# Performance work log

Measured on AMD Instinct MI355X. Metric: run time of the kernel, lower is better.

## Reference

```python
import jax, jax.numpy as jnp
import numpy as np
import math

B, D, L, Nh, Dk, Dv, K, CONV_NUM = 16, 256, 1024, 8, 32, 32, 7, 4
EPS = 1e-5


def _pos_encoding():
    # matches PosEncoder: freqs/phases per channel, sin(pos*freqs + phases), shape [D, L]
    idx = jnp.arange(D)
    i = idx.astype(jnp.float32)
    even = (idx % 2 == 0)
    freqs = jnp.where(even, 10000.0 ** (-i / D), -(10000.0 ** ((1.0 - i) / D)))
    phases = jnp.where(even, 0.0, math.pi / 2)
    pos = jnp.arange(L, dtype=jnp.float32)
    return jnp.sin(pos[None, :] * freqs[:, None] + phases[:, None])


def _layer_norm(x, g, b):
    # nn.LayerNorm([D, L]) on [B, D, L]: normalize over last two dims
    m = jnp.mean(x, axis=(1, 2), keepdims=True)
    v = jnp.mean((x - m) ** 2, axis=(1, 2), keepdims=True)
    return (x - m) * jax.lax.rsqrt(v + EPS) * g + b


def _ds_conv(x, dw, db, pw, pb):
    # depthwise conv1d (groups=D, same padding) + pointwise 1x1 conv
    y = jax.lax.conv_general_dilated(
        x, dw[:, None, :], window_strides=(1,), padding=[(K // 2, K // 2)],
        feature_group_count=D, dimension_numbers=('NCH', 'OIH', 'NCH'))
    y = y + db[None, :, None]
    return jnp.einsum('bdl,ed->bel', y, pw) + pb[None, :, None]


def setup_inputs() -> dict:
    key = jax.random.key(0)
    ks = jax.random.split(key, 12)

    def n(k, shape, scale):
        return jax.random.normal(k, shape, jnp.float32) * scale

    x = jax.random.normal(ks[0], (B, D, L), jnp.float32)
    mask = jax.random.randint(ks[1], (B, L), 0, 2).astype(jnp.int32)
    dw_w = n(ks[2], (CONV_NUM, D, K), 0.1)
    dw_b = jnp.zeros((CONV_NUM, D), jnp.float32)
    pw_w = n(ks[3], (CONV_NUM, D, D), 0.05)
    pw_b = jnp.zeros((CONV_NUM, D), jnp.float32)
    ln_g = jnp.ones((CONV_NUM + 2, D, L), jnp.float32)
    ln_b = jnp.zeros((CONV_NUM + 2, D, L), jnp.float32)
    Wq = n(ks[4], (Nh, D, Dk), 0.05)
    Wk = n(ks[5], (Nh, D, Dk), 0.05)
    Wv = n(ks[6], (Nh, D, Dv), 0.05)
    Wo = n(ks[7], (D, Dv * Nh), 0.05)
    fc_w = n(ks[8], (D, D), 0.05)
    fc_b = jnp.zeros((D,), jnp.float32)
    return dict(x=x, mask=mask, dw_w=dw_w, dw_b=dw_b, pw_w=pw_w, pw_b=pw_b,
                ln_g=ln_g, ln_b=ln_b, Wq=Wq, Wk=Wk, Wv=Wv, Wo=Wo,
                fc_w=fc_w, fc_b=fc_b)


def reference(x, mask, dw_w, dw_b, pw_w, pw_b, ln_g, ln_b, Wq, Wk, Wv, Wo, fc_w, fc_b):
    m = mask.astype(jnp.float32)  # [B, L]
    out = x + _pos_encoding()[None]
    res = out
    out = _layer_norm(out, ln_g[0], ln_b[0])
    for i in range(CONV_NUM):
        out = jax.nn.relu(_ds_conv(out, dw_w[i], dw_b[i], pw_w[i], pw_b[i])) + res
        # F.dropout in eval mode is identity
        res = out
        out = _layer_norm(out, ln_g[i + 1], ln_b[i + 1])
    # self attention (batched over heads instead of per-head loop; same math)
    xt = out.transpose(0, 2, 1)  # [B, L, D]
    q = jnp.einsum('bld,hdk->bhlk', xt, Wq)
    k = jnp.einsum('bld,hdk->bhlk', xt, Wk)
    v = jnp.einsum('bld,hdv->bhlv', xt, Wv)
    scores = jnp.einsum('bhqk,bhlk->bhql', q, k) * (1.0 / math.sqrt(Dk))
    hm = m[:, None, None, :]  # mask over key dim
    scores = scores * hm + (1.0 - hm) * (-1e30)
    attn = jax.nn.softmax(scores, axis=-1) * m[:, None, :, None]  # zero padded query rows
    heads = jnp.einsum('bhql,bhlv->bqhv', attn, v).reshape(B, L, Nh * Dv)  # head-major concat
    att_out = (heads @ Wo).transpose(0, 2, 1)  # [B, D, L]
    out = att_out + res
    res = out
    out = _layer_norm(out, ln_g[CONV_NUM + 1], ln_b[CONV_NUM + 1])
    out = jnp.einsum('bdl,ed->bel', out, fc_w) + fc_b[None, :, None]  # nn.Linear on [B,L,D]
    out = jax.nn.relu(out) + res
    return out
```

## Files before the change

kernel.cpp:

```cpp
#include <hip/hip_runtime.h>
#include <hip/hip_bf16.h>

#define NB 16
#define ND 256
#define NL 1024
#define NHH 8
#define NDK 32
#define NKW 7
#define NCONV 4
#define NPB (ND*NL)

constexpr float LN_EPS = 1e-5f;

typedef __attribute__((ext_vector_type(4))) float f32x4;
typedef __attribute__((ext_vector_type(4))) short bf16x4;
typedef __attribute__((ext_vector_type(8))) short bf16x8;

__device__ __forceinline__ short bf16s(float f){
  return (short)__builtin_bit_cast(unsigned short, __float2bfloat16(f));
}
__device__ __forceinline__ float b2f(short s){
  return __builtin_bit_cast(float, ((unsigned)(unsigned short)s) << 16);
}

__device__ __forceinline__ void ln_ab(const float* st, int slot, int b, float& mean, float& rstd){
  float s = 0.f, ss = 0.f;
  #pragma unroll
  for(int bin=0;bin<8;bin++){
    const float* p = st + ((size_t)((slot*NB+b)*8+bin))*32;
    s += p[0]; ss += p[1];
  }
  mean = s * (1.0f/NPB);
  float var = ss * (1.0f/NPB) - mean*mean;
  rstd = rsqrtf(var + LN_EPS);
}

__device__ __forceinline__ void stats_reduce(float s, float ss, float* stats, int slot, int b, int bin){
  __shared__ float red[8];
  #pragma unroll
  for(int o=32;o>0;o>>=1){ s += __shfl_down(s,o); ss += __shfl_down(ss,o); }
  int lane = threadIdx.x & 63, w = threadIdx.x >> 6;
  if(lane==0){ red[w*2]=s; red[w*2+1]=ss; }
  __syncthreads();
  if(threadIdx.x==0){
    float* p = stats + ((size_t)((slot*NB+b)*8+bin))*32;
    atomicAdd(&p[0], red[0]+red[2]+red[4]+red[6]);
    atomicAdd(&p[1], red[1]+red[3]+red[5]+red[7]);
  }
}

__global__ __launch_bounds__(256) void k_prep(const float* __restrict__ pw_w, const float* __restrict__ fc_w,
    const float* __restrict__ Wo, const float* __restrict__ Wq, const float* __restrict__ Wk,
    const float* __restrict__ Wv, const float* __restrict__ g, const float* __restrict__ btab,
    short* __restrict__ Wpwb, short* __restrict__ Wfcb, short* __restrict__ Wob, short* __restrict__ Wcat,
    short* __restrict__ gT, short* __restrict__ bT, float* __restrict__ postab){
  __shared__ float T[64][65];
  int blk = blockIdx.x, tid = threadIdx.x;
  if(blk < 256){
    int idx = blk*1024 + tid*4;
    f32x4 v = *(const f32x4*)(pw_w + idx);
    bf16x4 o;
    #pragma unroll
    for(int j=0;j<4;j++) o[j] = bf16s(v[j]);
    *(bf16x4*)(Wpwb + idx) = o;
  } else if(blk < 320){
    int idx = (blk-256)*1024 + tid*4;
    f32x4 v = *(const f32x4*)(fc_w + idx);
    bf16x4 o;
    #pragma unroll
    for(int j=0;j<4;j++) o[j] = bf16s(v[j]);
    *(bf16x4*)(Wfcb + idx) = o;
  } else if(blk < 384){
    int idx = (blk-320)*1024 + tid*4;
    int e = idx >> 8;
    bf16x4 o;
    #pragma unroll
    for(int j=0;j<4;j++){ int d = (idx+j)&255; o[j] = bf16s(Wo[d*ND + e]); }
    *(bf16x4*)(Wob + idx) = o;
  } else if(blk < 576){
    int idx = (blk-384)*1024 + tid*4;
    int og = idx >> 8, d = idx & 255;
    int seg = og >> 8, o = og & 255, h = o >> 5, k = o & 31;
    const float* W = (seg==0) ? Wq : ((seg==1) ? Wk : Wv);
    bf16x4 ov;
    #pragma unroll
    for(int j=0;j<4;j++) ov[j] = bf16s(W[((size_t)(h*ND + d + j))*NDK + k]);
    *(bf16x4*)(Wcat + idx) = ov;
  } else if(blk < 832){
    int d = blk - 576;
    int l = tid*4;
    const float LN1E4_OVER_D = 9.210340371976184f / (float)ND;
    float freq, phase;
    if((d & 1) == 0){ freq =  __expf(-(float)d*LN1E4_OVER_D);      phase = 0.f; }
    else            { freq = -__expf((1.f-(float)d)*LN1E4_OVER_D); phase = 1.5707963267948966f; }
    f32x4 o;
    #pragma unroll
    for(int j=0;j<4;j++) o[j] = sinf((float)(l+j)*freq + phase);
    *(f32x4*)(postab + ((size_t)d<<10) + l) = o;
  } else {
    int blk2 = blk - 832;
    int which = blk2 >> 6;
    int tile = blk2 & 63;
    int d0 = (tile & 3) << 6, l0 = (tile >> 2) << 6;
    const float* src = (which < 6) ? (g + (size_t)which*NPB) : (btab + (size_t)(which-6)*NPB);
    short* dst = (which < 6) ? (gT + (size_t)which*NPB) : (bT + (size_t)(which-6)*NPB);
    for(int i=tid;i<1024;i+=256){
      int dd = i>>4, l4 = i&15;
      f32x4 v = *(const f32x4*)(src + (size_t)(d0+dd)*NL + l0 + l4*4);
      #pragma unroll
      for(int j=0;j<4;j++) T[dd][l4*4+j] = v[j];
    }
    __syncthreads();
    for(int i=tid;i<1024;i+=256){
      int ll = i>>4, d4 = i&15;
      bf16x4 o;
      #pragma unroll
      for(int j=0;j<4;j++) o[j] = bf16s(T[d4*4+j][ll]);
      *(bf16x4*)(dst + (size_t)(l0+ll)*ND + d0 + d4*4) = o;
    }
  }
}

__global__ __launch_bounds__(256) void k_posadd(const float* __restrict__ x, const float* __restrict__ postab,
                                                short* __restrict__ Rb, float* __restrict__ stats){
  int blk = blockIdx.x;
  int lt = blk & 15, dt = (blk>>4)&3, b = blk>>6;
  int l0 = lt*64, d0 = dt*64;
  __shared__ float T[64][65];
  int tid = threadIdx.x;
  for(int i=tid;i<1024;i+=256){
    int dd = i>>4, l4 = i&15;
    int d = d0+dd;
    f32x4 xv = *(const f32x4*)(x + ((size_t)(b*ND+d)<<10) + l0 + l4*4);
    f32x4 pv = *(const f32x4*)(postab + ((size_t)d<<10) + l0 + l4*4);
    #pragma unroll
    for(int j=0;j<4;j++) T[dd][l4*4+j] = xv[j] + pv[j];
  }
  __syncthreads();
  float s=0.f, ss=0.f;
  for(int i=tid;i<1024;i+=256){
    int ll = i>>4, d4 = i&15;
    bf16x4 o;
    #pragma unroll
    for(int j=0;j<4;j++){
      short rs = bf16s(T[d4*4+j][ll]);
      o[j] = rs;
      float rv = b2f(rs);
      s += rv; ss += rv*rv;
    }
    *(bf16x4*)(Rb + ((size_t)(b*NL+l0+ll)<<8) + d0 + d4*4) = o;
  }
  stats_reduce(s, ss, stats, 0, b, blk & 7);
}

__global__ __launch_bounds__(256) void k_dwconvT(const short* __restrict__ Rb, const short* __restrict__ gT,
                                                 const short* __restrict__ bT, const float* __restrict__ w7,
                                                 const float* __restrict__ db, const float* __restrict__ stats,
                                                 short* __restrict__ Y, int slot){
  int blk = blockIdx.x;
  int lblk = blk & 63, b = blk >> 6;
  int tid = threadIdx.x;
  __shared__ float wLds[NKW][ND];
  __shared__ float dbLds[ND];
  for(int i=tid;i<ND*NKW;i+=256){ int d=i/NKW, q=i-d*NKW; wLds[q][d] = w7[i]; }
  dbLds[tid] = db[tid];
  float mean, rstd; ln_ab(stats, slot, b, mean, rstd);
  float mr = mean*rstd;
  __syncthreads();
  int d0 = (tid & 63)*4;
  int l0 = lblk*16 + (tid >> 6)*4;
  f32x4 ln[10];
  #pragma unroll
  for(int i=0;i<10;i++){
    int lp = l0 - 3 + i;
    if(lp >= 0 && lp < NL){
      bf16x4 v = *(const bf16x4*)(Rb + ((size_t)(b*NL+lp)<<8) + d0);
      bf16x4 gv = *(const bf16x4*)(gT + ((size_t)lp<<8) + d0);
      bf16x4 bv = *(const bf16x4*)(bT + ((size_t)lp<<8) + d0);
      f32x4 t;
      #pragma unroll
      for(int j=0;j<4;j++) t[j] = (b2f(v[j])*rstd - mr)*b2f(gv[j]) + b2f(bv[j]);
      ln[i] = t;
    } else ln[i] = (f32x4){0.f,0.f,0.f,0.f};
  }
  f32x4 dbv = *(const f32x4*)(&dbLds[d0]);
  #pragma unroll
  for(int jl=0;jl<4;jl++){
    f32x4 acc = dbv;
    #pragma unroll
    for(int q=0;q<NKW;q++){
      f32x4 wq = *(const f32x4*)(&wLds[q][d0]);
      #pragma unroll
      for(int j=0;j<4;j++) acc[j] += ln[jl+q][j]*wq[j];
    }
    bf16x4 o;
    #pragma unroll
    for(int j=0;j<4;j++) o[j] = bf16s(acc[j]);
    *(bf16x4*)(Y + ((size_t)(b*NL + l0 + jl)<<8) + d0) = o;
  }
}

__device__ __forceinline__ void stage_rows_bf16(short* dst, const short* src, int tid, int c){
  for(int i=tid;i<1024;i+=256){
    int rr = i>>4, kk = i&15;
    bf16x8 w = *(const bf16x8*)(src + (size_t)rr*ND + c*128 + kk*8);
    *(bf16x8*)((char*)dst + rr*256 + ((kk*16) ^ ((rr&7)<<4))) = w;
  }
}
__device__ __forceinline__ void stage_act_lnb(short* dst, const short* src, const short* g, const short* bt,
                                              float mean, float rstd, int tid, int c){
  float mr = mean*rstd;
  for(int i=tid;i<1024;i+=256){
    int ll = i>>4, kk = i&15;
    size_t off = (size_t)ll*ND + c*128 + kk*8;
    bf16x8 v = *(const bf16x8*)(src + off);
    bf16x8 gv = *(const bf16x8*)(g + off);
    bf16x8 bv = *(const bf16x8*)(bt + off);
    bf16x8 o;
    #pragma unroll
    for(int j=0;j<8;j++) o[j] = bf16s((b2f(v[j])*rstd - mr)*b2f(gv[j]) + b2f(bv[j]));
    *(bf16x8*)((char*)dst + ll*256 + ((kk*16) ^ ((ll&7)<<4))) = o;
  }
}
__device__ __forceinline__ void mfma_core(const short* As, const short* Bs, int wm, int wn,
                                          int lq, int gg, f32x4 acc[2][2]){
  #pragma unroll
  for(int t=0;t<4;t++){
    bf16x8 a[2], bb[2];
    #pragma unroll
    for(int m=0;m<2;m++){
      int row = wm*32 + m*16 + lq;
      a[m] = *(const bf16x8*)((const char*)As + row*256 + ((t*64 + gg*16) ^ ((row&7)<<4)));
    }
    #pragma unroll
    for(int n=0;n<2;n++){
      int row = wn*32 + n*16 + lq;
      bb[n] = *(const bf16x8*)((const char*)Bs + row*256 + ((t*64 + gg*16) ^ ((row&7)<<4)));
    }
    #pragma unroll
    for(int m=0;m<2;m++)
      #pragma unroll
      for(int n=0;n<2;n++)
        acc[m][n] = __builtin_amdgcn_mfma_f32_16x16x32_bf16(a[m], bb[n], acc[m][n], 0,0,0);
  }
}

#define GEMM_PROLOGUE() \
  int blk = blockIdx.x; \
  int lt = blk & 15, et = (blk>>4)&3, b = blk>>6; \
  int l0 = lt*64, e0 = et*64; \
  int tid = threadIdx.x; \
  int w = tid>>6, lane = tid&63, lq = lane&15, gg = lane>>4; \
  int wm = w&1, wn = w>>1; \
  __shared__ short As[8192], Bs[8192]; \
  f32x4 acc[2][2]; \
  acc[0][0]=acc[0][1]=acc[1][0]=acc[1][1] = (f32x4){0.f,0.f,0.f,0.f};

__global__ __launch_bounds__(256) void k_pw(const short* __restrict__ Y, const short* __restrict__ Wb,
                                            const float* __restrict__ bias, short* __restrict__ Rb,
                                            float* __restrict__ stats, int slot_out){
  GEMM_PROLOGUE();
  const short* Asrc = Y + ((size_t)(b*NL)+l0)*ND;
  const short* Bsrc = Wb + (size_t)e0*ND;
  for(int c=0;c<2;c++){
    __syncthreads();
    stage_rows_bf16(As, Asrc, tid, c);
    stage_rows_bf16(Bs, Bsrc, tid, c);
    __syncthreads();
    mfma_core(As, Bs, wm, wn, lq, gg, acc);
  }
  float s=0.f, ss=0.f;
  #pragma unroll
  for(int n=0;n<2;n++){
    int e = e0 + wn*32 + n*16 + lq;
    float bv = bias[e];
    #pragma unroll
    for(int m=0;m<2;m++){
      #pragma unroll
      for(int r=0;r<4;r++){
        int l = l0 + wm*32 + m*16 + gg*4 + r;
        size_t ix = (size_t)(b*NL+l)*ND + e;
        float v = fmaxf(acc[m][n][r] + bv, 0.f);
        float rr = b2f(Rb[ix]) + v;
        short rs = bf16s(rr);
        Rb[ix] = rs;
        float r2 = b2f(rs);
        s += r2; ss += r2*r2;
      }
    }
  }
  stats_reduce(s, ss, stats, slot_out, b, blk & 7);
}

__global__ __launch_bounds__(256) void k_qkvf(const short* __restrict__ Rb, const short* __restrict__ gT,
                                              const short* __restrict__ bT, const float* __restrict__ stats,
                                              const short* __restrict__ Wcat, short* __restrict__ Qb,
                                              short* __restrict__ Kb, short* __restrict__ Vb){
  int blk = blockIdx.x;
  int lt = blk & 15;
  int tmp = blk >> 4;
  int et = tmp % 12, b = tmp / 12;
  int l0 = lt*64, e0g = et*64;
  int seg = et >> 2;
  int tid = threadIdx.x;
  int w = tid>>6, lane = tid&63, lq = lane&15, gg = lane>>4;
  int wm = w&1, wn = w>>1;
  __shared__ short As[8192], Bs[8192];
  f32x4 acc[2][2];
  acc[0][0]=acc[0][1]=acc[1][0]=acc[1][1] = (f32x4){0.f,0.f,0.f,0.f};
  float mean, rstd; ln_ab(stats, 4, b, mean, rstd);
  const short* Asrc = Rb + ((size_t)(b*NL)+l0)*ND;
  const short* gs = gT + (size_t)l0*ND;
  const short* bs = bT + (size_t)l0*ND;
  const short* Bsrc = Wcat + (size_t)e0g*ND;
  for(int c=0;c<2;c++){
    __syncthreads();
    stage_act_lnb(As, Asrc, gs, bs, mean, rstd, tid, c);
    stage_rows_bf16(Bs, Bsrc, tid, c);
    __syncthreads();
    mfma_core(As, Bs, wm, wn, lq, gg, acc);
  }
  #pragma unroll
  for(int n=0;n<2;n++){
    int eo = (et&3)*64 + wn*32 + n*16 + lq;
    int h = eo>>5, dk = eo&31;
    if(seg < 2){
      short* outp = (seg==0) ? Qb : Kb;
      #pragma unroll
      for(int m=0;m<2;m++){
        #pragma unroll
        for(int r=0;r<4;r++){
          int l = l0 + wm*32 + m*16 + gg*4 + r;
          outp[((size_t)(b*NHH+h)*NL + l)*NDK + dk] = bf16s(acc[m][n][r]);
        }
      }
    } else {
      #pragma unroll
      for(int m=0;m<2;m++){
        int lb = l0 + wm*32 + m*16 + gg*4;
        bf16x4 pk;
        #pragma unroll
        for(int r=0;r<4;r++) pk[r] = bf16s(acc[m][n][r]);
        *(bf16x4*)(Vb + ((size_t)(b*NHH+h)*NDK + dk)*NL + lb) = pk;
      }
    }
  }
}

__global__ __launch_bounds__(256) void k_attn(const short* __restrict__ Qb, const short* __restrict__ Kb,
                                              const short* __restrict__ Vt, const int* __restrict__ mask,
                                              short* __restrict__ heads){
  int blk = blockIdx.x;
  int qblk = blk >> 7, bh = blk & 127;
  int b = bh >> 3, h = bh & 7;
  int tid = threadIdx.x;
  int w = tid >> 6, lane = tid & 63;
  int lq = lane & 15, gg = lane >> 4;

  __shared__ short Ks[64][40];
  __shared__ short Vs[32*64];
  __shared__ short Ps[4][16][40];
  __shared__ float msh[64];

  int qrow = qblk*64 + w*16 + lq;
  bf16x8 qf = *(const bf16x8*)(Qb + ((size_t)bh*NL + qrow)*NDK + gg*8);

  bf16x8 ones;
  #pragma unroll
  for(int j=0;j<8;j++) ones[j] = (short)0x3F80;

  f32x4 zero = {0.f,0.f,0.f,0.f};
  f32x4 o0 = zero, o1 = zero, o2 = zero;
  const float scale = 0.17677669529663687f;

  for(int t0=0; t0<NL; t0+=64){
    __syncthreads();
    {
      int key = tid >> 2, c = tid & 3;
      *(bf16x8*)(&Ks[key][c*8]) = *(const bf16x8*)(Kb + ((size_t)bh*NL + t0 + key)*NDK + c*8);
      int v = tid >> 3, ch = tid & 7;
      *(bf16x8*)((char*)Vs + v*128 + ((ch*16) ^ ((v&7)<<4))) =
          *(const bf16x8*)(Vt + ((size_t)bh*NDK + v)*NL + t0 + ch*8);
      if(tid < 64) msh[tid] = ((float)mask[b*NL + t0 + tid] - 1.f) * 1e30f;
    }
    __syncthreads();
    #pragma unroll
    for(int sub=0; sub<2; sub++){
      bf16x8 a0 = *(const bf16x8*)(&Ks[sub*32 + lq][gg*8]);
      bf16x8 a1 = *(const bf16x8*)(&Ks[sub*32 + 16 + lq][gg*8]);
      f32x4 c0 = __builtin_amdgcn_mfma_f32_16x16x32_bf16(a0, qf, zero, 0, 0, 0);
      f32x4 c1 = __builtin_amdgcn_mfma_f32_16x16x32_bf16(a1, qf, zero, 0, 0, 0);
      bf16x4 p0, p1;
      #pragma unroll
      for(int r=0;r<4;r++){
        float pv0 = __expf(__builtin_fmaf(c0[r], scale, msh[sub*32 + gg*4 + r]));
        p0[r] = bf16s(pv0);
        float pv1 = __expf(__builtin_fmaf(c1[r], scale, msh[sub*32 + 16 + gg*4 + r]));
        p1[r] = bf16s(pv1);
      }
      *(bf16x4*)(&Ps[w][lq][gg*4])      = p0;
      *(bf16x4*)(&Ps[w][lq][16 + gg*4]) = p1;
      bf16x8 pf = *(const bf16x8*)(&Ps[w][lq][gg*8]);
      int cc = sub*4 + gg;
      bf16x8 b0 = *(const bf16x8*)((const char*)Vs + lq*128      + ((cc*16) ^ ((lq&7)<<4)));
      bf16x8 b1 = *(const bf16x8*)((const char*)Vs + (16+lq)*128 + ((cc*16) ^ (((16+lq)&7)<<4)));
      o0 = __builtin_amdgcn_mfma_f32_16x16x32_bf16(pf, b0, o0, 0, 0, 0);
      o1 = __builtin_amdgcn_mfma_f32_16x16x32_bf16(pf, b1, o1, 0, 0, 0);
      o2 = __builtin_amdgcn_mfma_f32_16x16x32_bf16(pf, ones, o2, 0, 0, 0);
    }
  }
  #pragma unroll
  for(int r=0;r<4;r++){
    int ql = gg*4 + r;
    int qg = qblk*64 + w*16 + ql;
    float mq = (float)mask[b*NL + qg];
    float sc = mq / o2[r];
    short* op = heads + ((size_t)(b*NL + qg))*(NHH*NDK) + h*NDK;
    op[lq]      = bf16s(o0[r]*sc);
    op[16 + lq] = bf16s(o1[r]*sc);
  }
}

__global__ __launch_bounds__(256) void k_wo(const short* __restrict__ H, const short* __restrict__ Wb,
                                            short* __restrict__ Rb, float* __restrict__ stats){
  GEMM_PROLOGUE();
  const short* Asrc = H + ((size_t)(b*NL)+l0)*ND;
  const short* Bsrc = Wb + (size_t)e0*ND;
  for(int c=0;c<2;c++){
    __syncthreads();
    stage_rows_bf16(As, Asrc, tid, c);
    stage_rows_bf16(Bs, Bsrc, tid, c);
    __syncthreads();
    mfma_core(As, Bs, wm, wn, lq, gg, acc);
  }
  float s=0.f, ss=0.f;
  #pragma unroll
  for(int n=0;n<2;n++){
    int e = e0 + wn*32 + n*16 + lq;
    #pragma unroll
    for(int m=0;m<2;m++){
      #pragma unroll
      for(int r=0;r<4;r++){
        int l = l0 + wm*32 + m*16 + gg*4 + r;
        size_t ix = (size_t)(b*NL+l)*ND + e;
        float rr = b2f(Rb[ix]) + acc[m][n][r];
        short rs = bf16s(rr);
        Rb[ix] = rs;
        float r2 = b2f(rs);
        s += r2; ss += r2*r2;
      }
    }
  }
  stats_reduce(s, ss, stats, 5, b, blk & 7);
}

__global__ __launch_bounds__(256) void k_fc(const short* __restrict__ Rb, const short* __restrict__ gT,
                                            const short* __restrict__ bT, const float* __restrict__ stats,
                                            const short* __restrict__ Wb, const float* __restrict__ bias,
                                            float* __restrict__ out){
  GEMM_PROLOGUE();
  float mean, rstd; ln_ab(stats, 5, b, mean, rstd);
  const short* Asrc = Rb + ((size_t)(b*NL)+l0)*ND;
  const short* gs = gT + (size_t)l0*ND;
  const short* bs = bT + (size_t)l0*ND;
  const short* Bsrc = Wb + (size_t)e0*ND;
  for(int c=0;c<2;c++){
    __syncthreads();
    stage_act_lnb(As, Asrc, gs, bs, mean, rstd, tid, c);
    stage_rows_bf16(Bs, Bsrc, tid, c);
    __syncthreads();
    mfma_core(As, Bs, wm, wn, lq, gg, acc);
  }
  #pragma unroll
  for(int n=0;n<2;n++){
    int e = e0 + wn*32 + n*16 + lq;
    float bv = bias[e];
    #pragma unroll
    for(int m=0;m<2;m++){
      int lb = l0 + wm*32 + m*16 + gg*4;
      f32x4 ov;
      #pragma unroll
      for(int r=0;r<4;r++){
        float v = fmaxf(acc[m][n][r] + bv, 0.f);
        ov[r] = v + b2f(Rb[(size_t)(b*NL+lb+r)*ND + e]);
      }
      *(f32x4*)(out + (size_t)(b*ND+e)*NL + lb) = ov;
    }
  }
}

extern "C" void kernel_launch(void* const* d_in, const int* in_sizes, int n_in,
                              void* d_out, int out_size, void* d_ws, size_t ws_size,
                              hipStream_t stream){
  const float* x    = (const float*)d_in[0];
  const int*   mask = (const int*)d_in[1];
  const float* dw_w = (const float*)d_in[2];
  const float* dw_b = (const float*)d_in[3];
  const float* pw_w = (const float*)d_in[4];
  const float* pw_b = (const float*)d_in[5];
  const float* ln_g = (const float*)d_in[6];
  const float* ln_b = (const float*)d_in[7];
  const float* Wq   = (const float*)d_in[8];
  const float* Wk   = (const float*)d_in[9];
  const float* Wv   = (const float*)d_in[10];
  const float* Wo   = (const float*)d_in[11];
  const float* fc_w = (const float*)d_in[12];
  const float* fc_b = (const float*)d_in[13];

  float* ws     = (float*)d_ws;
  float* stats  = ws;
  float* postab = ws + 98304;
  short* Rb     = (short*)(ws + 360448);
  short* Yb     = (short*)(ws + 2457600);
  short* Hb     = (short*)(ws + 4554752);
  short* Qb     = (short*)(ws + 6651904);
  short* Kb     = (short*)(ws + 8749056);
  short* Vb     = (short*)(ws + 10846208);
  short* gT     = (short*)(ws + 12943360);
  short* bT     = (short*)(ws + 13729792);
  short* Wpwb   = (short*)(ws + 14516224);
  short* Wfcb   = (short*)(ws + 14647296);
  short* Wob    = (short*)(ws + 14680064);
  short* Wcat   = (short*)(ws + 14712832);

  hipMemsetAsync(stats, 0, 98304*sizeof(float), stream);
  k_prep<<<1600,256,0,stream>>>(pw_w, fc_w, Wo, Wq, Wk, Wv, ln_g, ln_b,
                                Wpwb, Wfcb, Wob, Wcat, gT, bT, postab);
  k_posadd<<<1024,256,0,stream>>>(x, postab, Rb, stats);
  for(int i=0;i<NCONV;i++){
    k_dwconvT<<<1024,256,0,stream>>>(Rb, gT + (size_t)i*NPB, bT + (size_t)i*NPB,
                                     dw_w + i*ND*NKW, dw_b + i*ND, stats, Yb, i);
    k_pw<<<1024,256,0,stream>>>(Yb, Wpwb + (size_t)i*65536, pw_b + i*ND, Rb, stats, i+1);
  }
  k_qkvf<<<3072,256,0,stream>>>(Rb, gT + (size_t)4*NPB, bT + (size_t)4*NPB, stats, Wcat, Qb, Kb, Vb);
  k_attn<<<2048,256,0,stream>>>(Qb, Kb, Vb, mask, Hb);
  k_wo<<<1024,256,0,stream>>>(Hb, Wob, Rb, stats);
  k_fc<<<1024,256,0,stream>>>(Rb, gT + (size_t)5*NPB, bT + (size_t)5*NPB, stats, Wfcb, fc_b, (float*)d_out);
}
```

Measured before the change: 299.5 us.

## Prefetch next tile into registers in GEMM and attention loops

Global loads for the next K-chunk (GEMM kernels) and the next key/value block (attention kernel) are issued into registers before the current tile's MFMA work. The register contents are then written to LDS at the top of the next iteration. This aims to hide global memory latency behind compute, at the cost of extra registers per thread. With only two chunks in the GEMMs the overlap available there is limited.

```diff
diff --git a/kernel.cpp b/kernel.cpp
--- a/kernel.cpp
+++ b/kernel.cpp
@@ -200,6 +200,38 @@
   }
 }
 
+__device__ __forceinline__ void load_rows_regs(bf16x8 r[4], const short* src, int tid, int c){
+  #pragma unroll
+  for(int it=0;it<4;it++){
+    int i = tid + it*256;
+    int rr = i>>4, kk = i&15;
+    r[it] = *(const bf16x8*)(src + (size_t)rr*ND + c*128 + kk*8);
+  }
+}
+__device__ __forceinline__ void write_rows_lds(short* dst, const bf16x8 r[4], int tid){
+  #pragma unroll
+  for(int it=0;it<4;it++){
+    int i = tid + it*256;
+    int rr = i>>4, kk = i&15;
+    *(bf16x8*)((char*)dst + rr*256 + ((kk*16) ^ ((rr&7)<<4))) = r[it];
+  }
+}
+__device__ __forceinline__ void write_act_lds(short* dst, const bf16x8 rv[4], const short* g, const short* bt,
+                                              float mean, float rstd, int tid, int c){
+  float mr = mean*rstd;
+  #pragma unroll
+  for(int it=0;it<4;it++){
+    int i = tid + it*256;
+    int ll = i>>4, kk = i&15;
+    size_t off = (size_t)ll*ND + c*128 + kk*8;
+    bf16x8 gv = *(const bf16x8*)(g + off);
+    bf16x8 bv = *(const bf16x8*)(bt + off);
+    bf16x8 o;
+    #pragma unroll
+    for(int j=0;j<8;j++) o[j] = bf16s((b2f(rv[it][j])*rstd - mr)*b2f(gv[j]) + b2f(bv[j]));
+    *(bf16x8*)((char*)dst + ll*256 + ((kk*16) ^ ((ll&7)<<4))) = o;
+  }
+}
 __device__ __forceinline__ void stage_rows_bf16(short* dst, const short* src, int tid, int c){
   for(int i=tid;i<1024;i+=256){
     int rr = i>>4, kk = i&15;
@@ -262,10 +294,15 @@
   GEMM_PROLOGUE();
   const short* Asrc = Y + ((size_t)(b*NL)+l0)*ND;
   const short* Bsrc = Wb + (size_t)e0*ND;
+  bf16x8 ra[4], rbw[4];
+  load_rows_regs(ra, Asrc, tid, 0);
+  load_rows_regs(rbw, Bsrc, tid, 0);
+  #pragma unroll
   for(int c=0;c<2;c++){
     __syncthreads();
-    stage_rows_bf16(As, Asrc, tid, c);
-    stage_rows_bf16(Bs, Bsrc, tid, c);
+    write_rows_lds(As, ra, tid);
+    write_rows_lds(Bs, rbw, tid);
+    if(c==0){ load_rows_regs(ra, Asrc, tid, 1); load_rows_regs(rbw, Bsrc, tid, 1); }
     __syncthreads();
     mfma_core(As, Bs, wm, wn, lq, gg, acc);
   }
@@ -373,15 +410,25 @@
   f32x4 o0 = zero, o1 = zero, o2 = zero;
   const float scale = 0.17677669529663687f;
 
+  const short* Kst = Kb + (size_t)bh*NL*NDK;
+  const short* Vst = Vt + (size_t)bh*NDK*NL;
+  int skey = tid >> 2, sc = tid & 3;
+  int sv = tid >> 3, sch = tid & 7;
+
+  bf16x8 kreg = *(const bf16x8*)(Kst + (size_t)skey*NDK + sc*8);
+  bf16x8 vreg = *(const bf16x8*)(Vst + (size_t)sv*NL + sch*8);
+  float mreg = 0.f;
+  if(tid < 64) mreg = ((float)mask[b*NL + tid] - 1.f) * 1e30f;
+
   for(int t0=0; t0<NL; t0+=64){
     __syncthreads();
-    {
-      int key = tid >> 2, c = tid & 3;
-      *(bf16x8*)(&Ks[key][c*8]) = *(const bf16x8*)(Kb + ((size_t)bh*NL + t0 + key)*NDK + c*8);
-      int v = tid >> 3, ch = tid & 7;
-      *(bf16x8*)((char*)Vs + v*128 + ((ch*16) ^ ((v&7)<<4))) =
-          *(const bf16x8*)(Vt + ((size_t)bh*NDK + v)*NL + t0 + ch*8);
-      if(tid < 64) msh[tid] = ((float)mask[b*NL + t0 + tid] - 1.f) * 1e30f;
+    *(bf16x8*)(&Ks[skey][sc*8]) = kreg;
+    *(bf16x8*)((char*)Vs + sv*128 + ((sch*16) ^ ((sv&7)<<4))) = vreg;
+    if(tid < 64) msh[tid] = mreg;
+    if(t0 + 64 < NL){
+      kreg = *(const bf16x8*)(Kst + (size_t)(t0 + 64 + skey)*NDK + sc*8);
+      vreg = *(const bf16x8*)(Vst + (size_t)sv*NL + t0 + 64 + sch*8);
+      if(tid < 64) mreg = ((float)mask[b*NL + t0 + 64 + tid] - 1.f) * 1e30f;
     }
     __syncthreads();
     #pragma unroll
@@ -414,10 +461,10 @@
     int ql = gg*4 + r;
     int qg = qblk*64 + w*16 + ql;
     float mq = (float)mask[b*NL + qg];
-    float sc = mq / o2[r];
+    float sc2 = mq / o2[r];
     short* op = heads + ((size_t)(b*NL + qg))*(NHH*NDK) + h*NDK;
-    op[lq]      = bf16s(o0[r]*sc);
-    op[16 + lq] = bf16s(o1[r]*sc);
+    op[lq]      = bf16s(o0[r]*sc2);
+    op[16 + lq] = bf16s(o1[r]*sc2);
   }
 }
 
@@ -426,10 +473,15 @@
   GEMM_PROLOGUE();
   const short* Asrc = H + ((size_t)(b*NL)+l0)*ND;
   const short* Bsrc = Wb + (size_t)e0*ND;
+  bf16x8 ra[4], rbw[4];
+  load_rows_regs(ra, Asrc, tid, 0);
+  load_rows_regs(rbw, Bsrc, tid, 0);
+  #pragma unroll
   for(int c=0;c<2;c++){
     __syncthreads();
-    stage_rows_bf16(As, Asrc, tid, c);
-    stage_rows_bf16(Bs, Bsrc, tid, c);
+    write_rows_lds(As, ra, tid);
+    write_rows_lds(Bs, rbw, tid);
+    if(c==0){ load_rows_regs(ra, Asrc, tid, 1); load_rows_regs(rbw, Bsrc, tid, 1); }
     __syncthreads();
     mfma_core(As, Bs, wm, wn, lq, gg, acc);
   }
@@ -464,10 +516,15 @@
   const short* gs = gT + (size_t)l0*ND;
   const short* bs = bT + (size_t)l0*ND;
   const short* Bsrc = Wb + (size_t)e0*ND;
+  bf16x8 rv[4], rbw[4];
+  load_rows_regs(rv, Asrc, tid, 0);
+  load_rows_regs(rbw, Bsrc, tid, 0);
+  #pragma unroll
   for(int c=0;c<2;c++){
     __syncthreads();
-    stage_act_lnb(As, Asrc, gs, bs, mean, rstd, tid, c);
-    stage_rows_bf16(Bs, Bsrc, tid, c);
+    write_act_lds(As, rv, gs, bs, mean, rstd, tid, c);
+    write_rows_lds(Bs, rbw, tid);
+    if(c==0){ load_rows_regs(rv, Asrc, tid, 1); load_rows_regs(rbw, Bsrc, tid, 1); }
     __syncthreads();
     mfma_core(As, Bs, wm, wn, lq, gg, acc);
   }
```

Result: faster. 288.3 us (-3.8%).
